# Kernel optimization log

Measured on AMD Instinct MI355X. Metric: run time of the kernel, lower is better.

The kernel has to match this reference:

```python
import jax, jax.numpy as jnp
import numpy as np

B, T = 256, 4096
L = 128          # shapelet_length
K = 128          # num_shapelets
K_TOP = 5


def setup_inputs() -> dict:
    key = jax.random.key(0)
    kx, ks = jax.random.split(key)
    x = jax.random.normal(kx, (B, T), dtype=jnp.float32)
    shapelets = jax.random.normal(ks, (K, L), dtype=jnp.float32) * 0.1
    return {"x": x, "shapelets": shapelets}


def reference(x, shapelets):
    # x: [B, T], shapelets: [K, L]
    N = x.shape[1] - L + 1  # number of sliding windows
    # Gather overlapping windows: x_win [B, N, L]
    idx = jnp.arange(N)[:, None] + jnp.arange(L)[None, :]
    x_win = x[:, idx]
    # Per-window mean removal
    x_norm = x_win - jnp.mean(x_win, axis=2, keepdims=True)
    # Per-shapelet mean removal
    s_norm = shapelets - jnp.mean(shapelets, axis=1, keepdims=True)
    # Correlation: [B, N, K]
    corr = jnp.einsum('bnl,kl->bnk', x_norm, s_norm)
    k_val = min(K_TOP, N)
    # top-k over window dim N -> move N to last axis
    topk_vals, _ = jax.lax.top_k(jnp.transpose(corr, (0, 2, 1)), k_val)  # [B, K, k]
    p1 = topk_vals[:, :, 0]
    p2 = topk_vals[:, :, 1] if k_val >= 2 else p1
    p_mean = jnp.mean(topk_vals, axis=2)
    dominance = jax.nn.relu(p1 - p2)
    return jnp.concatenate([p1, p_mean, p2, dominance], axis=1)  # [B, 4K]
```

## Files before the change

kernel.cpp:

```cpp
#include <hip/hip_runtime.h>

#define T_LEN 4096
#define N_WIN 3969
#define K_SH  128
#define L_SH  128
#define B_SZ  256

#define SSTR  136
#define XSTR  4360

typedef __attribute__((ext_vector_type(8))) __bf16 bf16x8;
typedef __attribute__((ext_vector_type(4))) float f32x4;
typedef _Float16 h2 __attribute__((ext_vector_type(2)));

__device__ __forceinline__ unsigned short f2bf(float f) {
    union { float f; unsigned int u; } c; c.f = f;
    unsigned int u = c.u + 0x7fff + ((c.u >> 16) & 1u);
    return (unsigned short)(u >> 16);
}
__device__ __forceinline__ unsigned int pack2(unsigned short lo, unsigned short hi) {
    return (unsigned int)lo | ((unsigned int)hi << 16);
}

__device__ __forceinline__ h2 max2(h2 a, h2 b) { return __builtin_elementwise_max(a, b); }
__device__ __forceinline__ h2 min2(h2 a, h2 b) { return __builtin_elementwise_min(a, b); }
__device__ __forceinline__ h2 cvt2(float lo, float hi) {
    return __builtin_bit_cast(h2, __builtin_amdgcn_cvt_pkrtz(lo, hi));
}
__device__ __forceinline__ void ce2(h2& hi, h2& lo) {
    const h2 m = max2(hi, lo);
    lo = min2(hi, lo);
    hi = m;
}
__device__ __forceinline__ void sort4_2(h2& a, h2& b, h2& c, h2& d) {
    ce2(a, b); ce2(c, d); ce2(a, c); ce2(b, d); ce2(b, c);
}
__device__ __forceinline__ void merge44_top5_2(h2 a0, h2 a1, h2 a2, h2 a3,
                                               h2 b0, h2 b1, h2 b2, h2 b3,
                                               h2& r0, h2& r1, h2& r2, h2& r3, h2& r4) {
    ce2(a0, b0); ce2(a2, b2); ce2(b0, a2);
    ce2(a1, b1); ce2(a3, b3); ce2(b1, a3);
    r0 = a0;
    r1 = a1; r2 = b0; ce2(r1, r2);
    r3 = b1; r4 = a2; ce2(r3, r4);
}
__device__ __forceinline__ void merge55_2(h2& r0, h2& r1, h2& r2, h2& r3, h2& r4,
                                          h2 s0, h2 s1, h2 s2, h2 s3, h2 s4) {
    const h2 m00 = min2(r0, s0);
    const h2 m10 = min2(r1, s0), m01 = min2(r0, s1);
    const h2 m20 = min2(r2, s0), m11 = min2(r1, s1), m02 = min2(r0, s2);
    const h2 m30 = min2(r3, s0), m21 = min2(r2, s1), m12 = min2(r1, s2), m03 = min2(r0, s3);
    const h2 n0 = max2(r0, s0);
    const h2 n1 = max2(max2(r1, s1), m00);
    const h2 n2 = max2(max2(r2, s2), max2(m10, m01));
    const h2 n3 = max2(max2(max2(r3, s3), m20), max2(m11, m02));
    const h2 n4 = max2(max2(max2(r4, s4), max2(m30, m03)), max2(m21, m12));
    r0 = n0; r1 = n1; r2 = n2; r3 = n3; r4 = n4;
}
__device__ __forceinline__ void insert1_2(h2 v, h2* rt) {
    h2 b = max2(rt[4], v); h2 m;
    m = max2(rt[3], b);     b     = min2(rt[3], b);     rt[3] = m;
    m = max2(rt[2], rt[3]); rt[3] = min2(rt[2], rt[3]); rt[2] = m;
    m = max2(rt[1], rt[2]); rt[2] = min2(rt[1], rt[2]); rt[1] = m;
    m = max2(rt[0], rt[1]); rt[1] = min2(rt[0], rt[1]); rt[0] = m;
    rt[4] = b;
}
__device__ __forceinline__ void select32(const f32x4* acc0, const f32x4* acc1, h2* rt) {
    h2 p[16];
    #pragma unroll
    for (int m = 0; m < 4; ++m)
        #pragma unroll
        for (int i = 0; i < 4; ++i)
            p[4 * m + i] = cvt2(acc0[m][i], acc1[m][i]);
    sort4_2(p[0], p[1], p[2],  p[3]);
    sort4_2(p[4], p[5], p[6],  p[7]);
    sort4_2(p[8], p[9], p[10], p[11]);
    sort4_2(p[12], p[13], p[14], p[15]);
    h2 u0, u1, u2, u3, u4, v0, v1, v2, v3, v4;
    merge44_top5_2(p[0], p[1], p[2],  p[3],  p[4],  p[5],  p[6],  p[7],  u0, u1, u2, u3, u4);
    merge44_top5_2(p[8], p[9], p[10], p[11], p[12], p[13], p[14], p[15], v0, v1, v2, v3, v4);
    merge55_2(u0, u1, u2, u3, u4, v0, v1, v2, v3, v4);
    merge55_2(rt[0], rt[1], rt[2], rt[3], rt[4], u0, u1, u2, u3, u4);
}

__global__ __launch_bounds__(1024)
void shapelet_fused_kernel(const float* __restrict__ x,
                           const float* __restrict__ s,
                           float* __restrict__ out) {
    __shared__ __align__(16) unsigned short ldsS[K_SH * SSTR];
    __shared__ __align__(16) unsigned short ldsX[8 * XSTR];

    const int t    = threadIdx.x;
    const int lane = t & 63;
    const int w    = t >> 6;
    const int r    = lane & 15;
    const int q    = lane >> 4;
    const int c7   = lane & 7;
    const int ub   = (lane >> 3) & 1;
    const int g    = w >> 3;
    const int w7   = w & 7;
    const int mh   = w7 >> 2;
    const int wp   = w7 & 3;
    const int mtb  = 4 * mh;
    const int b    = blockIdx.x;

    {
        const int k = t >> 3, e8 = t & 7;
        const float4* srow = (const float4*)(s + k * L_SH + e8 * 16);
        float4 v[4];
        float sum = 0.0f;
        #pragma unroll
        for (int j = 0; j < 4; ++j) {
            v[j] = srow[j];
            sum += (v[j].x + v[j].y) + (v[j].z + v[j].w);
        }
        sum += __shfl_xor(sum, 1);
        sum += __shfl_xor(sum, 2);
        sum += __shfl_xor(sum, 4);
        const float mean = sum * (1.0f / 128.0f);
        uint4* dst = (uint4*)((char*)ldsS + k * (SSTR * 2) + e8 * 32);
        #pragma unroll
        for (int j = 0; j < 2; ++j) {
            uint4 o;
            o.x = pack2(f2bf(v[2*j].x - mean),   f2bf(v[2*j].y - mean));
            o.y = pack2(f2bf(v[2*j].z - mean),   f2bf(v[2*j].w - mean));
            o.z = pack2(f2bf(v[2*j+1].x - mean), f2bf(v[2*j+1].y - mean));
            o.w = pack2(f2bf(v[2*j+1].z - mean), f2bf(v[2*j+1].w - mean));
            dst[j] = o;
        }
        if (e8 == 7) *(uint4*)((char*)ldsS + k * (SSTR * 2) + 256) = make_uint4(0,0,0,0);
    }

    {
        const float* __restrict__ xb = x + (size_t)b * T_LEN;
        const int a = t & 7;
        for (int i = (t >> 3); i < XSTR / 8; i += 128) {
            const int p0 = 8 * i;
            float xv[16];
            if (p0 + 16 <= T_LEN) {
                const float4* sp = (const float4*)(xb + p0);
                #pragma unroll
                for (int j = 0; j < 4; ++j) *(float4*)(xv + 4 * j) = sp[j];
            } else {
                #pragma unroll
                for (int j = 0; j < 16; ++j) {
                    const int gi = p0 + j;
                    xv[j] = (gi < T_LEN) ? xb[gi] : 0.0f;
                }
            }
            unsigned short bv[16];
            #pragma unroll
            for (int j = 0; j < 16; ++j) bv[j] = f2bf(xv[j]);
            uint4 o;
            o.x = pack2(bv[a],     bv[a + 1]);
            o.y = pack2(bv[a + 2], bv[a + 3]);
            o.z = pack2(bv[a + 4], bv[a + 5]);
            o.w = pack2(bv[a + 6], bv[a + 7]);
            *(uint4*)((char*)ldsX + a * (XSTR * 2) + 2 * p0) = o;
        }
    }
    __syncthreads();

    bf16x8 bfr[2][4];
    #pragma unroll
    for (int kk = 0; kk < 2; ++kk)
        #pragma unroll
        for (int c = 0; c < 4; ++c)
            bfr[kk][c] = __builtin_bit_cast(bf16x8, *(const uint4*)(
                (const char*)ldsS + ((2 * wp + kk) * 16 + r) * (SSTR * 2) + 64 * c + 16 * q));

    h2 rt[5];
    #pragma unroll
    for (int i = 0; i < 5; ++i) rt[i] = __builtin_bit_cast(h2, 0xFC00FC00u);

    const char* xp = (const char*)ldsX + c7 * (XSTR * 2) + 16 * q + 16 * ub + 32 * mtb
                   + g * 256;

#define TILE_STEP                                                               \
    {                                                                           \
        bf16x8 afr[10];                                                         \
        _Pragma("unroll")                                                       \
        for (int j = 0; j < 10; ++j)                                            \
            afr[j] = __builtin_bit_cast(bf16x8, *(const uint4*)(xp + 32 * j));  \
        xp += 512;                                                              \
        f32x4 acc0[4], acc1[4];                                                 \
        _Pragma("unroll")                                                       \
        for (int m = 0; m < 4; ++m) {                                           \
            acc0[m] = (f32x4){0.f, 0.f, 0.f, 0.f};                              \
            acc1[m] = (f32x4){0.f, 0.f, 0.f, 0.f};                              \
        }                                                                       \
        _Pragma("unroll")                                                       \
        for (int c = 0; c < 4; ++c) {                                           \
            _Pragma("unroll")                                                   \
            for (int m = 0; m < 4; ++m) {                                       \
                acc0[m] = __builtin_amdgcn_mfma_f32_16x16x32_bf16(afr[m + 2*c], bfr[0][c], acc0[m], 0, 0, 0); \
                acc1[m] = __builtin_amdgcn_mfma_f32_16x16x32_bf16(afr[m + 2*c], bfr[1][c], acc1[m], 0, 0, 0); \
            }                                                                   \
        }                                                                       \
        select32(acc0, acc1, rt);                                               \
    }

    for (int st = 0; st < 15; ++st) { TILE_STEP }
    if (g == 0) { TILE_STEP }
#undef TILE_STEP

    if (g == 1 && mh == 0) {
        f32x4 e0 = (f32x4){0.f, 0.f, 0.f, 0.f};
        f32x4 e1 = (f32x4){0.f, 0.f, 0.f, 0.f};
        const char* eb = (const char*)ldsX + c7 * (XSTR * 2) + 7936 + 16 * q + 16 * ub;
        #pragma unroll
        for (int c = 0; c < 4; ++c) {
            const bf16x8 af = __builtin_bit_cast(bf16x8, *(const uint4*)(eb + 64 * c));
            e0 = __builtin_amdgcn_mfma_f32_16x16x32_bf16(af, bfr[0][c], e0, 0, 0, 0);
            e1 = __builtin_amdgcn_mfma_f32_16x16x32_bf16(af, bfr[1][c], e1, 0, 0, 0);
        }
        if (q == 0) insert1_2(cvt2(e0[0], e1[0]), rt);
    }

    #pragma unroll
    for (int mask = 16; mask <= 32; mask <<= 1) {
        h2 sv[5];
        #pragma unroll
        for (int i = 0; i < 5; ++i)
            sv[i] = __builtin_bit_cast(h2, __shfl_xor(__builtin_bit_cast(int, rt[i]), mask));
        merge55_2(rt[0], rt[1], rt[2], rt[3], rt[4], sv[0], sv[1], sv[2], sv[3], sv[4]);
    }

    __syncthreads();
    unsigned int* pbuf = (unsigned int*)ldsS;
    if ((g != 0 || mh != 0) && q == 0) {
        const int reg = (g * 2 + mh) - 1;
        unsigned int* p = pbuf + ((reg * 64) + wp * 16 + r) * 5;
        #pragma unroll
        for (int i = 0; i < 5; ++i) p[i] = __builtin_bit_cast(unsigned int, rt[i]);
    }
    __syncthreads();
    if (g == 0 && mh == 0 && q == 0) {
        #pragma unroll
        for (int reg = 0; reg < 3; ++reg) {
            const unsigned int* p = pbuf + ((reg * 64) + wp * 16 + r) * 5;
            h2 sv[5];
            #pragma unroll
            for (int i = 0; i < 5; ++i) sv[i] = __builtin_bit_cast(h2, p[i]);
            merge55_2(rt[0], rt[1], rt[2], rt[3], rt[4], sv[0], sv[1], sv[2], sv[3], sv[4]);
        }

        const float A0 = (float)rt[0][0], A1 = (float)rt[1][0], A2 = (float)rt[2][0],
                    A3 = (float)rt[3][0], A4 = (float)rt[4][0];
        const float B0 = (float)rt[0][1], B1 = (float)rt[1][1], B2 = (float)rt[2][1],
                    B3 = (float)rt[3][1], B4 = (float)rt[4][1];
        float* ob = out + (size_t)b * (4 * K_SH);
        const int ksA = 32 * wp + r, ksB = ksA + 16;
        const float mA = (((A0 + A1) + (A2 + A3)) + A4) * 0.2f;
        const float mB = (((B0 + B1) + (B2 + B3)) + B4) * 0.2f;
        ob[ksA]           = A0;
        ob[K_SH + ksA]    = mA;
        ob[2*K_SH + ksA]  = A1;
        ob[3*K_SH + ksA]  = fmaxf(A0 - A1, 0.0f);
        ob[ksB]           = B0;
        ob[K_SH + ksB]    = mB;
        ob[2*K_SH + ksB]  = B1;
        ob[3*K_SH + ksB]  = fmaxf(B0 - B1, 0.0f);
    }
}

extern "C" void kernel_launch(void* const* d_in, const int* in_sizes, int n_in,
                              void* d_out, int out_size, void* d_ws, size_t ws_size,
                              hipStream_t stream) {
    const float* x = (const float*)d_in[0];
    const float* s = (const float*)d_in[1];
    float* out = (float*)d_out;
    shapelet_fused_kernel<<<B_SZ, 1024, 0, stream>>>(x, s, out);
}
```

Measured before the change: 93.31 us.

## Split shapelets across two blocks per batch row and share one LDS buffer

Launches two blocks per batch row, each handling half of the shapelets. Each block's waves now cover more window groups with fewer tile steps each. The shapelet and x staging share a single LDS buffer, so per-block LDS use drops, which could allow more resident blocks. Each x row is now converted and staged twice, and the final reduction merges 8 partial top-5 lists instead of 4. The first MFMA of each tile also takes a zero accumulator directly instead of separate zero-initialisation.

Measured after the change: 119.0 us. +27.5%, slower.

```diff
diff --git a/kernel.cpp b/kernel.cpp
--- a/kernel.cpp
+++ b/kernel.cpp
@@ -83,12 +83,11 @@
     merge55_2(rt[0], rt[1], rt[2], rt[3], rt[4], u0, u1, u2, u3, u4);
 }
 
-__global__ __launch_bounds__(1024)
-void shapelet_fused_kernel(const float* __restrict__ x,
-                           const float* __restrict__ s,
-                           float* __restrict__ out) {
-    __shared__ __align__(16) unsigned short ldsS[K_SH * SSTR];
-    __shared__ __align__(16) unsigned short ldsX[8 * XSTR];
+__global__ __launch_bounds__(1024, 8)
+void shapelet_ksplit_kernel(const float* __restrict__ x,
+                            const float* __restrict__ s,
+                            float* __restrict__ out) {
+    __shared__ __align__(16) unsigned short ldsU[8 * XSTR];
 
     const int t    = threadIdx.x;
     const int lane = t & 63;
@@ -97,39 +96,43 @@
     const int q    = lane >> 4;
     const int c7   = lane & 7;
     const int ub   = (lane >> 3) & 1;
-    const int g    = w >> 3;
     const int w7   = w & 7;
     const int mh   = w7 >> 2;
-    const int wp   = w7 & 3;
+    const int G    = 2 * (w >> 3) + ((w7 >> 1) & 1);
+    const int wp   = w7 & 1;
     const int mtb  = 4 * mh;
-    const int b    = blockIdx.x;
+    const int bid  = blockIdx.x;
+    const int b    = bid >> 1;
+    const int kh   = bid & 1;
 
     {
-        const int k = t >> 3, e8 = t & 7;
-        const float4* srow = (const float4*)(s + k * L_SH + e8 * 16);
-        float4 v[4];
-        float sum = 0.0f;
-        #pragma unroll
-        for (int j = 0; j < 4; ++j) {
-            v[j] = srow[j];
-            sum += (v[j].x + v[j].y) + (v[j].z + v[j].w);
-        }
+        const int kl = t >> 4;
+        const int e  = t & 15;
+        const float4* srow = (const float4*)(s + (kh * 64 + kl) * L_SH + e * 8);
+        const float4 v0 = srow[0], v1 = srow[1];
+        float sum = ((v0.x + v0.y) + (v0.z + v0.w)) + ((v1.x + v1.y) + (v1.z + v1.w));
         sum += __shfl_xor(sum, 1);
         sum += __shfl_xor(sum, 2);
         sum += __shfl_xor(sum, 4);
+        sum += __shfl_xor(sum, 8);
         const float mean = sum * (1.0f / 128.0f);
-        uint4* dst = (uint4*)((char*)ldsS + k * (SSTR * 2) + e8 * 32);
-        #pragma unroll
-        for (int j = 0; j < 2; ++j) {
-            uint4 o;
-            o.x = pack2(f2bf(v[2*j].x - mean),   f2bf(v[2*j].y - mean));
-            o.y = pack2(f2bf(v[2*j].z - mean),   f2bf(v[2*j].w - mean));
-            o.z = pack2(f2bf(v[2*j+1].x - mean), f2bf(v[2*j+1].y - mean));
-            o.w = pack2(f2bf(v[2*j+1].z - mean), f2bf(v[2*j+1].w - mean));
-            dst[j] = o;
-        }
-        if (e8 == 7) *(uint4*)((char*)ldsS + k * (SSTR * 2) + 256) = make_uint4(0,0,0,0);
-    }
+        uint4 o;
+        o.x = pack2(f2bf(v0.x - mean), f2bf(v0.y - mean));
+        o.y = pack2(f2bf(v0.z - mean), f2bf(v0.w - mean));
+        o.z = pack2(f2bf(v1.x - mean), f2bf(v1.y - mean));
+        o.w = pack2(f2bf(v1.z - mean), f2bf(v1.w - mean));
+        *(uint4*)((char*)ldsU + kl * (SSTR * 2) + e * 16) = o;
+    }
+    __syncthreads();
+
+    bf16x8 bfr[2][4];
+    #pragma unroll
+    for (int kk = 0; kk < 2; ++kk)
+        #pragma unroll
+        for (int c = 0; c < 4; ++c)
+            bfr[kk][c] = __builtin_bit_cast(bf16x8, *(const uint4*)(
+                (const char*)ldsU + ((2 * wp + kk) * 16 + r) * (SSTR * 2) + 64 * c + 16 * q));
+    __syncthreads();
 
     {
         const float* __restrict__ xb = x + (size_t)b * T_LEN;
@@ -156,25 +159,19 @@
             o.y = pack2(bv[a + 2], bv[a + 3]);
             o.z = pack2(bv[a + 4], bv[a + 5]);
             o.w = pack2(bv[a + 6], bv[a + 7]);
-            *(uint4*)((char*)ldsX + a * (XSTR * 2) + 2 * p0) = o;
+            *(uint4*)((char*)ldsU + a * (XSTR * 2) + 2 * p0) = o;
         }
     }
     __syncthreads();
 
-    bf16x8 bfr[2][4];
-    #pragma unroll
-    for (int kk = 0; kk < 2; ++kk)
-        #pragma unroll
-        for (int c = 0; c < 4; ++c)
-            bfr[kk][c] = __builtin_bit_cast(bf16x8, *(const uint4*)(
-                (const char*)ldsS + ((2 * wp + kk) * 16 + r) * (SSTR * 2) + 64 * c + 16 * q));
-
     h2 rt[5];
     #pragma unroll
     for (int i = 0; i < 5; ++i) rt[i] = __builtin_bit_cast(h2, 0xFC00FC00u);
 
-    const char* xp = (const char*)ldsX + c7 * (XSTR * 2) + 16 * q + 16 * ub + 32 * mtb
-                   + g * 256;
+    const char* xp = (const char*)ldsU + c7 * (XSTR * 2) + 16 * q + 16 * ub + 32 * mtb
+                   + G * 256;
+
+    const f32x4 ZCC = (f32x4){0.f, 0.f, 0.f, 0.f};
 
 #define TILE_STEP                                                               \
     {                                                                           \
@@ -182,15 +179,15 @@
         _Pragma("unroll")                                                       \
         for (int j = 0; j < 10; ++j)                                            \
             afr[j] = __builtin_bit_cast(bf16x8, *(const uint4*)(xp + 32 * j));  \
-        xp += 512;                                                              \
+        xp += 1024;                                                             \
         f32x4 acc0[4], acc1[4];                                                 \
         _Pragma("unroll")                                                       \
         for (int m = 0; m < 4; ++m) {                                           \
-            acc0[m] = (f32x4){0.f, 0.f, 0.f, 0.f};                              \
-            acc1[m] = (f32x4){0.f, 0.f, 0.f, 0.f};                              \
+            acc0[m] = __builtin_amdgcn_mfma_f32_16x16x32_bf16(afr[m], bfr[0][0], ZCC, 0, 0, 0); \
+            acc1[m] = __builtin_amdgcn_mfma_f32_16x16x32_bf16(afr[m], bfr[1][0], ZCC, 0, 0, 0); \
         }                                                                       \
         _Pragma("unroll")                                                       \
-        for (int c = 0; c < 4; ++c) {                                           \
+        for (int c = 1; c < 4; ++c) {                                           \
             _Pragma("unroll")                                                   \
             for (int m = 0; m < 4; ++m) {                                       \
                 acc0[m] = __builtin_amdgcn_mfma_f32_16x16x32_bf16(afr[m + 2*c], bfr[0][c], acc0[m], 0, 0, 0); \
@@ -200,14 +197,14 @@
         select32(acc0, acc1, rt);                                               \
     }
 
-    for (int st = 0; st < 15; ++st) { TILE_STEP }
-    if (g == 0) { TILE_STEP }
+    const int nst = (G < 3) ? 8 : 7;
+    for (int st = 0; st < nst; ++st) { TILE_STEP }
 #undef TILE_STEP
 
-    if (g == 1 && mh == 0) {
+    if (G == 3 && mh == 0) {
         f32x4 e0 = (f32x4){0.f, 0.f, 0.f, 0.f};
         f32x4 e1 = (f32x4){0.f, 0.f, 0.f, 0.f};
-        const char* eb = (const char*)ldsX + c7 * (XSTR * 2) + 7936 + 16 * q + 16 * ub;
+        const char* eb = (const char*)ldsU + c7 * (XSTR * 2) + 7936 + 16 * q + 16 * ub;
         #pragma unroll
         for (int c = 0; c < 4; ++c) {
             const bf16x8 af = __builtin_bit_cast(bf16x8, *(const uint4*)(eb + 64 * c));
@@ -227,18 +224,18 @@
     }
 
     __syncthreads();
-    unsigned int* pbuf = (unsigned int*)ldsS;
-    if ((g != 0 || mh != 0) && q == 0) {
-        const int reg = (g * 2 + mh) - 1;
-        unsigned int* p = pbuf + ((reg * 64) + wp * 16 + r) * 5;
+    unsigned int* pbuf = (unsigned int*)ldsU;
+    const int idx = 2 * G + mh;
+    if (idx != 0 && q == 0) {
+        unsigned int* p = pbuf + (((idx - 1) * 32) + wp * 16 + r) * 5;
         #pragma unroll
         for (int i = 0; i < 5; ++i) p[i] = __builtin_bit_cast(unsigned int, rt[i]);
     }
     __syncthreads();
-    if (g == 0 && mh == 0 && q == 0) {
-        #pragma unroll
-        for (int reg = 0; reg < 3; ++reg) {
-            const unsigned int* p = pbuf + ((reg * 64) + wp * 16 + r) * 5;
+    if (idx == 0 && q == 0) {
+        #pragma unroll
+        for (int reg = 0; reg < 7; ++reg) {
+            const unsigned int* p = pbuf + ((reg * 32) + wp * 16 + r) * 5;
             h2 sv[5];
             #pragma unroll
             for (int i = 0; i < 5; ++i) sv[i] = __builtin_bit_cast(h2, p[i]);
@@ -250,7 +247,7 @@
         const float B0 = (float)rt[0][1], B1 = (float)rt[1][1], B2 = (float)rt[2][1],
                     B3 = (float)rt[3][1], B4 = (float)rt[4][1];
         float* ob = out + (size_t)b * (4 * K_SH);
-        const int ksA = 32 * wp + r, ksB = ksA + 16;
+        const int ksA = kh * 64 + 32 * wp + r, ksB = ksA + 16;
         const float mA = (((A0 + A1) + (A2 + A3)) + A4) * 0.2f;
         const float mB = (((B0 + B1) + (B2 + B3)) + B4) * 0.2f;
         ob[ksA]           = A0;
@@ -270,5 +267,5 @@
     const float* x = (const float*)d_in[0];
     const float* s = (const float*)d_in[1];
     float* out = (float*)d_out;
-    shapelet_fused_kernel<<<B_SZ, 1024, 0, stream>>>(x, s, out);
-}
+    shapelet_ksplit_kernel<<<2 * B_SZ, 1024, 0, stream>>>(x, s, out);
+}
```
